# Kernel tuning notes

Hardware: AMD Instinct MI355X
Metric: run time of the kernel (lower is better)

The kernel has to match this reference:

```python
import jax, jax.numpy as jnp
import numpy as np

EPS = 1e-5
KS = 3
PAD = 1


def _bn(x, g, b, m, v):
    inv = g / jnp.sqrt(v + EPS)
    return x * inv[None, :, None, None] + (b - m * inv)[None, :, None, None]


def _deform_conv2d(x, off_w, off_b, w):
    # x: (B,C,H,W); off_w: (2*9,C,3,3); w: (Cout,C,3,3)
    B, C, H, W = x.shape
    N = KS * KS
    off = jax.lax.conv_general_dilated(x, off_w, (1, 1), ((PAD, PAD), (PAD, PAD)))
    off = off + off_b[None, :, None, None]                      # (B,2N,H,W)
    xp = jnp.pad(x, ((0, 0), (0, 0), (PAD, PAD), (PAD, PAD)))
    Hp, Wp = H + 2 * PAD, W + 2 * PAD
    r = jnp.arange(KS, dtype=x.dtype) - (KS - 1) // 2           # kernel offsets
    pny = jnp.repeat(r, KS)                                     # row-major (dy)
    pnx = jnp.tile(r, KS)                                       # row-major (dx)
    p0y = jnp.arange(1, H + 1, dtype=x.dtype)[None, None, :, None]
    p0x = jnp.arange(1, W + 1, dtype=x.dtype)[None, None, None, :]
    py = off[:, :N] + pny[None, :, None, None] + p0y            # (B,N,H,W)
    px = off[:, N:] + pnx[None, :, None, None] + p0x
    py = jnp.clip(py, 0.0, Hp - 1.0)
    px = jnp.clip(px, 0.0, Wp - 1.0)
    fy = jax.lax.stop_gradient(jnp.floor(py))                   # indices detached (as in torch impl)
    fx = jax.lax.stop_gradient(jnp.floor(px))
    qy0 = jnp.clip(fy, 0.0, Hp - 1.0)
    qx0 = jnp.clip(fx, 0.0, Wp - 1.0)
    qy1 = jnp.clip(fy + 1.0, 0.0, Hp - 1.0)
    qx1 = jnp.clip(fx + 1.0, 0.0, Wp - 1.0)
    xf = xp.reshape(B, C, Hp * Wp)

    def gather(qy, qx):
        idx = (qy * Wp + qx).astype(jnp.int32)                  # (B,N,H,W)
        return jax.vmap(lambda m_, i_: m_[:, i_])(xf, idx)       # (B,C,N,H,W)

    g_lt = (1.0 + (qy0 - py)) * (1.0 + (qx0 - px))
    g_rb = (1.0 - (qy1 - py)) * (1.0 - (qx1 - px))
    g_lb = (1.0 + (qy0 - py)) * (1.0 - (qx1 - px))
    g_rt = (1.0 - (qy1 - py)) * (1.0 + (qx0 - px))
    xo = (g_lt[:, None] * gather(qy0, qx0) + g_rb[:, None] * gather(qy1, qx1)
          + g_lb[:, None] * gather(qy0, qx1) + g_rt[:, None] * gather(qy1, qx0))
    # (B,C,N,H,W) -> (B,C,H*KS,W*KS): N = (row, col) row-major
    xo = xo.reshape(B, C, KS, KS, H, W).transpose(0, 1, 4, 2, 5, 3).reshape(B, C, H * KS, W * KS)
    return jax.lax.conv_general_dilated(xo, w, (KS, KS), 'VALID')


def _forward(x, dc1_offw, dc1_offb, dc1_w, bn1_g, bn1_b, bn1_m, bn1_v,
             dc2_offw, dc2_offb, dc2_w, bn2_g, bn2_b, bn2_m, bn2_v,
             id_w, id_b, bn3_g, bn3_b, bn3_m, bn3_v):
    h = jax.nn.relu(_bn(_deform_conv2d(x, dc1_offw, dc1_offb, dc1_w), bn1_g, bn1_b, bn1_m, bn1_v))
    h = _bn(_deform_conv2d(h, dc2_offw, dc2_offb, dc2_w), bn2_g, bn2_b, bn2_m, bn2_v)
    idt = jnp.einsum('bchw,oc->bohw', x, id_w[:, :, 0, 0]) + id_b[None, :, None, None]
    idt = _bn(idt, bn3_g, bn3_b, bn3_m, bn3_v)
    return jax.nn.relu(h + idt)


def setup_inputs() -> dict:
    key = jax.random.key(0)
    ks = jax.random.split(key, 16)
    B, Cin, Cout, H, W = 2, 64, 128, 128, 128
    N2 = 2 * KS * KS
    d = {}
    d['x'] = jax.random.normal(ks[0], (B, Cin, H, W), jnp.float32)
    d['dc1_offw'] = jax.random.normal(ks[1], (N2, Cin, KS, KS), jnp.float32) * 0.01
    d['dc1_offb'] = jnp.zeros((N2,), jnp.float32)
    d['dc1_w'] = jax.random.normal(ks[2], (Cout, Cin, KS, KS), jnp.float32) * 0.05
    d['bn1_g'] = 1.0 + 0.1 * jax.random.normal(ks[3], (Cout,), jnp.float32)
    d['bn1_b'] = 0.1 * jax.random.normal(ks[4], (Cout,), jnp.float32)
    d['bn1_m'] = 0.1 * jax.random.normal(ks[5], (Cout,), jnp.float32)
    d['bn1_v'] = jnp.ones((Cout,), jnp.float32)
    d['dc2_offw'] = jax.random.normal(ks[6], (N2, Cout, KS, KS), jnp.float32) * 0.01
    d['dc2_offb'] = jnp.zeros((N2,), jnp.float32)
    d['dc2_w'] = jax.random.normal(ks[7], (Cout, Cout, KS, KS), jnp.float32) * 0.03
    d['bn2_g'] = 1.0 + 0.1 * jax.random.normal(ks[8], (Cout,), jnp.float32)
    d['bn2_b'] = 0.1 * jax.random.normal(ks[9], (Cout,), jnp.float32)
    d['bn2_m'] = 0.1 * jax.random.normal(ks[10], (Cout,), jnp.float32)
    d['bn2_v'] = jnp.ones((Cout,), jnp.float32)
    d['id_w'] = jax.random.normal(ks[11], (Cout, Cin, 1, 1), jnp.float32) * 0.1
    d['id_b'] = jnp.zeros((Cout,), jnp.float32)
    d['bn3_g'] = 1.0 + 0.1 * jax.random.normal(ks[12], (Cout,), jnp.float32)
    d['bn3_b'] = 0.1 * jax.random.normal(ks[13], (Cout,), jnp.float32)
    d['bn3_m'] = 0.1 * jax.random.normal(ks[14], (Cout,), jnp.float32)
    d['bn3_v'] = jnp.ones((Cout,), jnp.float32)
    return d


def reference(x, dc1_offw, dc1_offb, dc1_w, bn1_g, bn1_b, bn1_m, bn1_v,
              dc2_offw, dc2_offb, dc2_w, bn2_g, bn2_b, bn2_m, bn2_v,
              id_w, id_b, bn3_g, bn3_b, bn3_m, bn3_v):
    return _forward(x, dc1_offw, dc1_offb, dc1_w, bn1_g, bn1_b, bn1_m, bn1_v,
                    dc2_offw, dc2_offb, dc2_w, bn2_g, bn2_b, bn2_m, bn2_v,
                    id_w, id_b, bn3_g, bn3_b, bn3_m, bn3_v)
```

## Files before the change

kernel.cpp:

```cpp
#include <hip/hip_runtime.h>
#include <math.h>

#define HH 128
#define WW 128
#define HWSZ (HH * WW)
#define BB 2
#define COUT 128

typedef __bf16 bf16x8 __attribute__((ext_vector_type(8)));
typedef float f32x4 __attribute__((ext_vector_type(4)));
typedef float f32x2 __attribute__((ext_vector_type(2)));
typedef short s16x8 __attribute__((ext_vector_type(8)));
typedef short s16x4 __attribute__((ext_vector_type(4)));
typedef unsigned short u16x4 __attribute__((ext_vector_type(4)));
typedef unsigned short u16x8 __attribute__((ext_vector_type(8)));

__device__ __forceinline__ short tobf(float f) {
  union { float f; unsigned u; } v; v.f = f;
  unsigned r = v.u + 0x7fffu + ((v.u >> 16) & 1u);
  return (short)(r >> 16);
}
__device__ __forceinline__ float asf(unsigned u) {
  union { unsigned u; float f; } v; v.u = u;
  return v.f;
}
__device__ __forceinline__ f32x2 up2(unsigned u) {
  f32x2 r; r[0] = asf(u << 16); r[1] = asf(u & 0xffff0000u); return r;
}
__device__ __forceinline__ unsigned pack2bf(float a, float b) {
  union { float f; unsigned u; } x, y; x.f = a; y.f = b;
  unsigned lo = (x.u + 0x7fffu + ((x.u >> 16) & 1u)) >> 16;
  unsigned hi = (y.u + 0x7fffu + ((y.u >> 16) & 1u)) & 0xffff0000u;
  return lo | hi;
}

#define PA0 73728
#define PA1 221184
#define PA2 229376
#define PA3 247808
#define PA4 284672
#define PA5 284928
__global__ __launch_bounds__(256) void prep_all_kernel(
    const float* __restrict__ dc1_w, const float* __restrict__ dc2_w,
    const float* __restrict__ id_w, const float* __restrict__ dc1_offw,
    const float* __restrict__ dc2_offw,
    const float* g1, const float* b1, const float* m1, const float* v1,
    const float* g2, const float* b2, const float* m2, const float* v2,
    const float* g3, const float* b3, const float* m3, const float* v3,
    const float* idb,
    short* __restrict__ wbf1, short* __restrict__ wbf2,
    short* __restrict__ woff1, short* __restrict__ woff2,
    float* __restrict__ cb1, float* __restrict__ cb2) {
  int idx = blockIdx.x * 256 + threadIdx.x;
  if (idx < PA0) {
    int o = idx / 576, k = idx - o * 576;
    float inv = g1[o] / sqrtf(v1[o] + 1e-5f);
    int col = (k % 9) * 64 + k / 9;
    wbf1[o * 576 + col] = tobf(dc1_w[(size_t)o * 576 + k] * inv);
  } else if (idx < PA1) {
    int j = idx - PA0;
    int o = j / 1152, k = j - o * 1152;
    float inv = g2[o] / sqrtf(v2[o] + 1e-5f);
    int col = (k % 9) * 128 + k / 9;
    wbf2[o * 1216 + col] = tobf(dc2_w[(size_t)o * 1152 + k] * inv);
  } else if (idx < PA2) {
    int j = idx - PA1;
    int o = j >> 6, k = j & 63;
    float inv = g3[o] / sqrtf(v3[o] + 1e-5f);
    wbf2[o * 1216 + 1152 + k] = tobf(id_w[(size_t)o * 64 + k] * inv);
  } else if (idx < PA3) {
    int j = idx - PA2;
    int o = j / 576, k = j - o * 576;
    int col = (k % 9) * 64 + k / 9;
    woff1[o * 576 + col] = (o < 18) ? tobf(dc1_offw[(size_t)o * 576 + k]) : (short)0;
  } else if (idx < PA4) {
    int j = idx - PA3;
    int o = j / 1152, k = j - o * 1152;
    int col = (k % 9) * 128 + k / 9;
    woff2[o * 1152 + col] = (o < 18) ? tobf(dc2_offw[(size_t)o * 1152 + k]) : (short)0;
  } else if (idx < PA5) {
    int j = idx - PA4;
    if (j < 128) {
      float inv = g1[j] / sqrtf(v1[j] + 1e-5f);
      cb1[j] = b1[j] - m1[j] * inv;
    } else {
      int o = j - 128;
      float inv2_ = g2[o] / sqrtf(v2[o] + 1e-5f);
      float inv3_ = g3[o] / sqrtf(v3[o] + 1e-5f);
      cb2[o] = (b2[o] - m2[o] * inv2_) + idb[o] * inv3_ + (b3[o] - m3[o] * inv3_);
    }
  }
}

__global__ __launch_bounds__(256) void xcast_kernel(const float* __restrict__ x,
                                                    unsigned short* __restrict__ xn) {
  __shared__ short lds[64 * 72];
  int tid = threadIdx.x;
  int gp0 = blockIdx.x * 64;
  int b = gp0 >> 14;
  int pl0 = gp0 & 16383;
  int p = tid & 63;
  int cb = (tid >> 6) * 16;
#pragma unroll
  for (int i = 0; i < 16; i++) {
    int c = cb + i;
    lds[p * 72 + c] = tobf(x[((size_t)(b * 64 + c)) * HWSZ + pl0 + p]);
  }
  __syncthreads();
  int pw = tid >> 2, cseg = (tid & 3) * 16;
  u16x8 a = *(const u16x8*)&lds[pw * 72 + cseg];
  u16x8 b8 = *(const u16x8*)&lds[pw * 72 + cseg + 8];
  *(u16x8*)&xn[(size_t)(gp0 + pw) * 64 + cseg] = a;
  *(u16x8*)&xn[(size_t)(gp0 + pw) * 64 + cseg + 8] = b8;
}

__global__ __launch_bounds__(256, 8) void offconv_mfma_kernel(
    const unsigned short* __restrict__ in, const short* __restrict__ woff,
    const float* __restrict__ offb, float* __restrict__ off, int cshift) {
  __shared__ short wlds[2][32 * 40];
  __shared__ short vlds[2][32 * 40];
  const int tid = threadIdx.x;
  const int lane = tid & 63, wv = tid >> 6;
  const int pb = ((blockIdx.x & 7) << 7) | (blockIdx.x >> 3);
  const int pix0 = pb << 5;
  const int x0 = pix0 & 127, y = (pix0 >> 7) & 127, b = pix0 >> 14;
  const int Cin = 1 << cshift;
  const int Kc = 9 << cshift;
  const unsigned short* inb = in + (size_t)b * HWSZ * Cin;
  const int ps = tid >> 3, cq = tid & 7;
  const int l15 = lane & 15, quad = lane >> 4;
  const int ptile = wv & 1, otile = wv >> 1;

  s16x8 wreg;
  u16x4 pk;
  auto issue = [&](int k0) {
    if (tid < 128) wreg = *(const s16x8*)&woff[(size_t)(tid >> 2) * Kc + k0 + (tid & 3) * 8];
    int n = k0 >> cshift;
    int dy = n / 3 - 1, dx = n % 3 - 1;
    int yy = y + dy;
    int xx = x0 + ps + dx;
    int c0 = (k0 & (Cin - 1)) + cq * 4;
    pk = (u16x4){0, 0, 0, 0};
    if (((unsigned)yy < (unsigned)HH) && ((unsigned)xx < (unsigned)WW))
      pk = *(const u16x4*)&inb[((size_t)yy * WW + xx) * Cin + c0];
  };
  auto commit = [&](int buf) {
    if (tid < 128) *(s16x8*)&wlds[buf][(tid >> 2) * 40 + (tid & 3) * 8] = wreg;
    *(u16x4*)&vlds[buf][ps * 40 + cq * 4] = pk;
  };

  f32x4 acc = {0.f, 0.f, 0.f, 0.f};
  issue(0);
  commit(0);
  __syncthreads();
  const int NC = Kc >> 5;
  for (int ch = 0; ch < NC; ch++) {
    int cur = ch & 1;
    bool has = (ch + 1) < NC;
    if (has) issue((ch + 1) << 5);
    bf16x8 bfr = *(const bf16x8*)&vlds[cur][(ptile * 16 + l15) * 40 + quad * 8];
    bf16x8 afr = *(const bf16x8*)&wlds[cur][(otile * 16 + l15) * 40 + quad * 8];
    acc = __builtin_amdgcn_mfma_f32_16x16x32_bf16(afr, bfr, acc, 0, 0, 0);
    if (has) commit(cur ^ 1);
    __syncthreads();
  }
#pragma unroll
  for (int r = 0; r < 4; r++) {
    int o = otile * 16 + quad * 4 + r;
    if (o < 18)
      off[(size_t)(b * 18 + o) * HWSZ + y * WW + x0 + ptile * 16 + l15] = acc[r] + offb[o];
  }
}

__global__ __launch_bounds__(512, 4) void deform_mfma_kernel(
    const unsigned short* __restrict__ in, const float* __restrict__ off,
    const short* __restrict__ wbf, const float* __restrict__ cbv,
    const unsigned short* __restrict__ xid, float* __restrict__ outf,
    unsigned short* __restrict__ outb, int cshift, int KCONV, int KTOT, int mode) {
  __shared__ __align__(16) char smem[49152];
  float4* dw = (float4*)smem;
  int4* da = (int4*)(smem + 9216);
  short* wlds = (short*)(smem + 18432);
  short* vlds = (short*)(smem + 38912);
  short* trans = (short*)smem;

  const int tid = threadIdx.x;
  const int lane = tid & 63, wv = tid >> 6;
  const int pb = ((blockIdx.x & 7) << 6) | (blockIdx.x >> 3);
  const int pix0 = pb << 6;
  const int x0 = pix0 & 127, y = (pix0 >> 7) & 127, b = pix0 >> 14;
  const int Cin = 1 << cshift;
  const unsigned short* inb = in + (size_t)b * HWSZ * Cin;
  const int ps = tid >> 3, cq = tid & 7;
  const int l15 = lane & 15, quad = lane >> 4;
  const int ptile = wv & 3, og = wv >> 2;

  for (int t = tid; t < 576; t += 512) {
    int n = t >> 6, pp = t & 63;
    float offy = off[(size_t)(b * 18 + n) * HWSZ + y * WW + x0 + pp];
    float offx = off[(size_t)(b * 18 + 9 + n) * HWSZ + y * WW + x0 + pp];
    float py = offy + (float)(n / 3 - 1) + (float)(y + 1);
    float px = offx + (float)(n % 3 - 1) + (float)(x0 + pp + 1);
    py = fminf(fmaxf(py, 0.f), 129.f);
    px = fminf(fmaxf(px, 0.f), 129.f);
    float fy = floorf(py), fx = floorf(px);
    float qy1 = fminf(fy + 1.f, 129.f), qx1 = fminf(fx + 1.f, 129.f);
    float ty0 = 1.f + fy - py, ty1 = 1.f - (qy1 - py);
    float tx0 = 1.f + fx - px, tx1 = 1.f - (qx1 - px);
    int iy0 = (int)fy - 1, ix0 = (int)fx - 1;
    int iy1 = (int)qy1 - 1, ix1 = (int)qx1 - 1;
    if ((unsigned)iy0 >= (unsigned)HH) ty0 = 0.f;
    if ((unsigned)iy1 >= (unsigned)HH) ty1 = 0.f;
    if ((unsigned)ix0 >= (unsigned)WW) tx0 = 0.f;
    if ((unsigned)ix1 >= (unsigned)WW) tx1 = 0.f;
    int by0 = min(max(iy0, 0), HH - 1), by1 = min(max(iy1, 0), HH - 1);
    int bx0 = min(max(ix0, 0), WW - 1), bx1 = min(max(ix1, 0), WW - 1);
    dw[t] = make_float4(ty0 * tx0, ty0 * tx1, ty1 * tx0, ty1 * tx1);
    da[t] = make_int4((by0 * WW + bx0) * Cin, (bx1 - bx0) * Cin,
                      (by1 - by0) * WW * Cin, 0);
  }

  f32x4 acc[4];
#pragma unroll
  for (int i = 0; i < 4; i++) acc[i] = (f32x4){0.f, 0.f, 0.f, 0.f};

  s16x8 wreg;
  uint2 t00, t01, t10, t11, pkr;
  float4 wgt;
  int isres = 0;

  auto issue = [&](int k0) {
    wreg = *(const s16x8*)&wbf[(size_t)(tid >> 2) * KTOT + k0 + (tid & 3) * 8];
    if (k0 < KCONV) {
      isres = 0;
      int n = k0 >> cshift;
      int c0 = (k0 & (Cin - 1)) + cq * 4;
      int d = (n << 6) + ps;
      wgt = dw[d];
      int4 a = da[d];
      const unsigned short* ptr = inb + a.x + c0;
      t00 = *(const uint2*)(ptr);
      t01 = *(const uint2*)(ptr + a.y);
      t10 = *(const uint2*)(ptr + a.z);
      t11 = *(const uint2*)(ptr + a.y + a.z);
    } else {
      isres = 1;
      int c = k0 - KCONV + cq * 4;
      pkr = *(const uint2*)&xid[((size_t)(b * HWSZ) + y * WW + x0 + ps) * 64 + c];
    }
  };
  auto commit = [&](int buf) {
    uint2 pk;
    if (!isres) {
      f32x2 v0 = up2(t00.x) * wgt.x + up2(t01.x) * wgt.y
               + up2(t10.x) * wgt.z + up2(t11.x) * wgt.w;
      f32x2 v1 = up2(t00.y) * wgt.x + up2(t01.y) * wgt.y
               + up2(t10.y) * wgt.z + up2(t11.y) * wgt.w;
      pk.x = pack2bf(v0[0], v0[1]);
      pk.y = pack2bf(v1[0], v1[1]);
    } else {
      pk = pkr;
    }
    *(s16x8*)&wlds[buf * 5120 + (tid >> 2) * 40 + (tid & 3) * 8] = wreg;
    *(uint2*)&vlds[buf * 2560 + ps * 40 + cq * 4] = pk;
  };

  __syncthreads();
  issue(0);
  commit(0);
  __syncthreads();
  const int NC = KTOT >> 5;
  for (int ch = 0; ch < NC; ch++) {
    int cur = ch & 1;
    bool has = (ch + 1) < NC;
    if (has) issue((ch + 1) << 5);
    bf16x8 bfr = *(const bf16x8*)&vlds[cur * 2560 + (ptile * 16 + l15) * 40 + quad * 8];
#pragma unroll
    for (int ot = 0; ot < 4; ot++) {
      bf16x8 afr = *(const bf16x8*)&wlds[cur * 5120 + (og * 64 + ot * 16 + l15) * 40 + quad * 8];
      acc[ot] = __builtin_amdgcn_mfma_f32_16x16x32_bf16(afr, bfr, acc[ot], 0, 0, 0);
    }
    if (has) commit(cur ^ 1);
    __syncthreads();
  }

  if (mode == 1) {
    int px_ = x0 + ptile * 16 + l15;
#pragma unroll
    for (int ot = 0; ot < 4; ot++) {
#pragma unroll
      for (int r = 0; r < 4; r++) {
        int o = og * 64 + ot * 16 + quad * 4 + r;
        outf[(size_t)(b * COUT + o) * HWSZ + y * WW + px_] =
            fmaxf(acc[ot][r] + cbv[o], 0.f);
      }
    }
  } else {
    int pl = ptile * 16 + l15;
#pragma unroll
    for (int ot = 0; ot < 4; ot++) {
      s16x4 t4;
#pragma unroll
      for (int r = 0; r < 4; r++) {
        int o = og * 64 + ot * 16 + quad * 4 + r;
        t4[r] = tobf(fmaxf(acc[ot][r] + cbv[o], 0.f));
      }
      *(s16x4*)&trans[pl * 136 + og * 64 + ot * 16 + quad * 4] = t4;
    }
    __syncthreads();
    int pw = tid >> 3, cseg = (tid & 7) * 16;
    u16x8 a = *(const u16x8*)&trans[pw * 136 + cseg];
    u16x8 b8 = *(const u16x8*)&trans[pw * 136 + cseg + 8];
    size_t gb = ((size_t)(b * HWSZ) + y * WW + x0 + pw) * 128 + cseg;
    *(u16x8*)&outb[gb] = a;
    *(u16x8*)&outb[gb + 8] = b8;
  }
}

extern "C" void kernel_launch(void* const* d_in, const int* in_sizes, int n_in,
                              void* d_out, int out_size, void* d_ws, size_t ws_size,
                              hipStream_t stream) {
  const float* x        = (const float*)d_in[0];
  const float* dc1_offw = (const float*)d_in[1];
  const float* dc1_offb = (const float*)d_in[2];
  const float* dc1_w    = (const float*)d_in[3];
  const float* bn1_g    = (const float*)d_in[4];
  const float* bn1_b    = (const float*)d_in[5];
  const float* bn1_m    = (const float*)d_in[6];
  const float* bn1_v    = (const float*)d_in[7];
  const float* dc2_offw = (const float*)d_in[8];
  const float* dc2_offb = (const float*)d_in[9];
  const float* dc2_w    = (const float*)d_in[10];
  const float* bn2_g    = (const float*)d_in[11];
  const float* bn2_b    = (const float*)d_in[12];
  const float* bn2_m    = (const float*)d_in[13];
  const float* bn2_v    = (const float*)d_in[14];
  const float* id_w     = (const float*)d_in[15];
  const float* id_b     = (const float*)d_in[16];
  const float* bn3_g    = (const float*)d_in[17];
  const float* bn3_b    = (const float*)d_in[18];
  const float* bn3_m    = (const float*)d_in[19];
  const float* bn3_v    = (const float*)d_in[20];

  float* wsf = (float*)d_ws;
  float* off1 = wsf;
  float* off2 = off1 + (size_t)BB * 18 * HWSZ;
  float* cb1  = off2 + (size_t)BB * 18 * HWSZ;
  float* cb2  = cb1 + 128;
  unsigned short* xbf = (unsigned short*)(cb2 + 128);
  unsigned short* h1  = xbf + (size_t)BB * HWSZ * 64;
  short* wbf1  = (short*)(h1 + (size_t)BB * HWSZ * COUT);
  short* wbf2  = wbf1 + (size_t)128 * 576;
  short* woff1 = wbf2 + (size_t)128 * 1216;
  short* woff2 = woff1 + (size_t)32 * 576;

  const int K1 = 576, K2 = 1152, KT2 = 1216;

  hipLaunchKernelGGL(prep_all_kernel, dim3((PA5 + 255) / 256), dim3(256), 0, stream,
                     dc1_w, dc2_w, id_w, dc1_offw, dc2_offw,
                     bn1_g, bn1_b, bn1_m, bn1_v, bn2_g, bn2_b, bn2_m, bn2_v,
                     bn3_g, bn3_b, bn3_m, bn3_v, id_b,
                     wbf1, wbf2, woff1, woff2, cb1, cb2);
  hipLaunchKernelGGL(xcast_kernel, dim3(BB * HWSZ / 64), dim3(256), 0, stream, x, xbf);

  hipLaunchKernelGGL(offconv_mfma_kernel, dim3(1024), dim3(256), 0, stream,
                     xbf, woff1, dc1_offb, off1, 6);
  hipLaunchKernelGGL(deform_mfma_kernel, dim3(512), dim3(512), 0, stream,
                     xbf, off1, wbf1, cb1, (const unsigned short*)nullptr,
                     (float*)nullptr, h1, 6, K1, K1, 0);
  hipLaunchKernelGGL(offconv_mfma_kernel, dim3(1024), dim3(256), 0, stream,
                     h1, woff2, dc2_offb, off2, 7);
  hipLaunchKernelGGL(deform_mfma_kernel, dim3(512), dim3(512), 0, stream,
                     h1, off2, wbf2, cb2, xbf, (float*)d_out,
                     (unsigned short*)nullptr, 7, K2, KT2, 1);
}
```

Measured before the change: 195.7 us.

## Restructure offset conv with split-K and deform conv with full-row tiles

The offset conv kernel now reads weights directly from global memory in a pre-swizzled MFMA fragment layout and reads activations straight into registers, with no LDS staging. It splits K across two wave groups that are combined through a single LDS reduction. The deform conv kernel now processes a full 128-pixel row per block with 8-channel vector gathers, stores the bilinear weights as bf16 and the deltas as packed int2 to save LDS, and prefetches two stages ahead. This roughly doubles data reuse per block and cuts per-chunk synchronisation, but raises register use (launch bounds drop to 2 blocks per CU), halves the grid, and rounds the bilinear weights to bf16.

```diff
diff --git a/kernel.cpp b/kernel.cpp
--- a/kernel.cpp
+++ b/kernel.cpp
@@ -27,8 +27,8 @@
 __device__ __forceinline__ f32x2 up2(unsigned u) {
   f32x2 r; r[0] = asf(u << 16); r[1] = asf(u & 0xffff0000u); return r;
 }
-__device__ __forceinline__ unsigned pack2bf(float a, float b) {
-  union { float f; unsigned u; } x, y; x.f = a; y.f = b;
+__device__ __forceinline__ unsigned pack2bf(f32x2 v) {
+  union { float f; unsigned u; } x, y; x.f = v[0]; y.f = v[1];
   unsigned lo = (x.u + 0x7fffu + ((x.u >> 16) & 1u)) >> 16;
   unsigned hi = (y.u + 0x7fffu + ((y.u >> 16) & 1u)) & 0xffff0000u;
   return lo | hi;
@@ -72,12 +72,16 @@
     int j = idx - PA2;
     int o = j / 576, k = j - o * 576;
     int col = (k % 9) * 64 + k / 9;
-    woff1[o * 576 + col] = (o < 18) ? tobf(dc1_offw[(size_t)o * 576 + k]) : (short)0;
+    int di = ((col >> 5) * 2 + (o >> 4)) * 512 + ((col >> 3) & 3) * 128
+           + (o & 15) * 8 + (col & 7);
+    woff1[di] = (o < 18) ? tobf(dc1_offw[(size_t)o * 576 + k]) : (short)0;
   } else if (idx < PA4) {
     int j = idx - PA3;
     int o = j / 1152, k = j - o * 1152;
     int col = (k % 9) * 128 + k / 9;
-    woff2[o * 1152 + col] = (o < 18) ? tobf(dc2_offw[(size_t)o * 1152 + k]) : (short)0;
+    int di = ((col >> 5) * 2 + (o >> 4)) * 512 + ((col >> 3) & 3) * 128
+           + (o & 15) * 8 + (col & 7);
+    woff2[di] = (o < 18) ? tobf(dc2_offw[(size_t)o * 1152 + k]) : (short)0;
   } else if (idx < PA5) {
     int j = idx - PA4;
     if (j < 128) {
@@ -114,93 +118,90 @@
   *(u16x8*)&xn[(size_t)(gp0 + pw) * 64 + cseg + 8] = b8;
 }
 
-__global__ __launch_bounds__(256, 8) void offconv_mfma_kernel(
+__global__ __launch_bounds__(512, 4) void offconv_mfma_kernel(
     const unsigned short* __restrict__ in, const short* __restrict__ woff,
     const float* __restrict__ offb, float* __restrict__ off, int cshift) {
-  __shared__ short wlds[2][32 * 40];
-  __shared__ short vlds[2][32 * 40];
+  __shared__ float redf[4 * 64 * 8];
   const int tid = threadIdx.x;
   const int lane = tid & 63, wv = tid >> 6;
-  const int pb = ((blockIdx.x & 7) << 7) | (blockIdx.x >> 3);
-  const int pix0 = pb << 5;
+  const int pxg = wv & 3, kh = wv >> 2;
+  const int pb = ((blockIdx.x & 7) << 6) | (blockIdx.x >> 3);
+  const int pix0 = pb << 6;
   const int x0 = pix0 & 127, y = (pix0 >> 7) & 127, b = pix0 >> 14;
   const int Cin = 1 << cshift;
-  const int Kc = 9 << cshift;
+  const int HK = (9 << cshift) >> 1;
+  const int NCh = HK >> 5;
   const unsigned short* inb = in + (size_t)b * HWSZ * Cin;
-  const int ps = tid >> 3, cq = tid & 7;
   const int l15 = lane & 15, quad = lane >> 4;
-  const int ptile = wv & 1, otile = wv >> 1;
-
-  s16x8 wreg;
-  u16x4 pk;
-  auto issue = [&](int k0) {
-    if (tid < 128) wreg = *(const s16x8*)&woff[(size_t)(tid >> 2) * Kc + k0 + (tid & 3) * 8];
+  const int px = x0 + pxg * 16 + l15;
+
+  f32x4 acc[2];
+  acc[0] = (f32x4){0.f, 0.f, 0.f, 0.f};
+  acc[1] = (f32x4){0.f, 0.f, 0.f, 0.f};
+
+  for (int i = 0; i < NCh; i++) {
+    int k0 = kh * HK + i * 32;
     int n = k0 >> cshift;
-    int dy = n / 3 - 1, dx = n % 3 - 1;
-    int yy = y + dy;
-    int xx = x0 + ps + dx;
-    int c0 = (k0 & (Cin - 1)) + cq * 4;
-    pk = (u16x4){0, 0, 0, 0};
+    int c0 = (k0 & (Cin - 1)) + quad * 8;
+    int yy = y + n / 3 - 1;
+    int xx = px + n % 3 - 1;
+    bf16x8 bv = {};
     if (((unsigned)yy < (unsigned)HH) && ((unsigned)xx < (unsigned)WW))
-      pk = *(const u16x4*)&inb[((size_t)yy * WW + xx) * Cin + c0];
-  };
-  auto commit = [&](int buf) {
-    if (tid < 128) *(s16x8*)&wlds[buf][(tid >> 2) * 40 + (tid & 3) * 8] = wreg;
-    *(u16x4*)&vlds[buf][ps * 40 + cq * 4] = pk;
-  };
-
-  f32x4 acc = {0.f, 0.f, 0.f, 0.f};
-  issue(0);
-  commit(0);
+      bv = *(const bf16x8*)&inb[((size_t)yy * WW + xx) * Cin + c0];
+    int fbase = (k0 >> 5) * 1024 + lane * 8;
+    bf16x8 a0 = *(const bf16x8*)&woff[fbase];
+    bf16x8 a1 = *(const bf16x8*)&woff[fbase + 512];
+    acc[0] = __builtin_amdgcn_mfma_f32_16x16x32_bf16(a0, bv, acc[0], 0, 0, 0);
+    acc[1] = __builtin_amdgcn_mfma_f32_16x16x32_bf16(a1, bv, acc[1], 0, 0, 0);
+  }
+  if (kh == 1) {
+    *(f32x4*)&redf[(pxg * 64 + lane) * 8] = acc[0];
+    *(f32x4*)&redf[(pxg * 64 + lane) * 8 + 4] = acc[1];
+  }
   __syncthreads();
-  const int NC = Kc >> 5;
-  for (int ch = 0; ch < NC; ch++) {
-    int cur = ch & 1;
-    bool has = (ch + 1) < NC;
-    if (has) issue((ch + 1) << 5);
-    bf16x8 bfr = *(const bf16x8*)&vlds[cur][(ptile * 16 + l15) * 40 + quad * 8];
-    bf16x8 afr = *(const bf16x8*)&wlds[cur][(otile * 16 + l15) * 40 + quad * 8];
-    acc = __builtin_amdgcn_mfma_f32_16x16x32_bf16(afr, bfr, acc, 0, 0, 0);
-    if (has) commit(cur ^ 1);
-    __syncthreads();
-  }
-#pragma unroll
-  for (int r = 0; r < 4; r++) {
-    int o = otile * 16 + quad * 4 + r;
-    if (o < 18)
-      off[(size_t)(b * 18 + o) * HWSZ + y * WW + x0 + ptile * 16 + l15] = acc[r] + offb[o];
-  }
-}
-
-__global__ __launch_bounds__(512, 4) void deform_mfma_kernel(
+  if (kh == 0) {
+    acc[0] += *(const f32x4*)&redf[(pxg * 64 + lane) * 8];
+    acc[1] += *(const f32x4*)&redf[(pxg * 64 + lane) * 8 + 4];
+#pragma unroll
+    for (int ot = 0; ot < 2; ot++) {
+#pragma unroll
+      for (int r = 0; r < 4; r++) {
+        int o = ot * 16 + quad * 4 + r;
+        if (o < 18)
+          off[(size_t)(b * 18 + o) * HWSZ + y * WW + px] = acc[ot][r] + offb[o];
+      }
+    }
+  }
+}
+
+__global__ __launch_bounds__(512, 2) void deform_mfma_kernel(
     const unsigned short* __restrict__ in, const float* __restrict__ off,
     const short* __restrict__ wbf, const float* __restrict__ cbv,
     const unsigned short* __restrict__ xid, float* __restrict__ outf,
     unsigned short* __restrict__ outb, int cshift, int KCONV, int KTOT, int mode) {
-  __shared__ __align__(16) char smem[49152];
-  float4* dw = (float4*)smem;
-  int4* da = (int4*)(smem + 9216);
+  __shared__ __align__(16) char smem[59392];
+  u16x4* dsw = (u16x4*)smem;
+  int2* dsa = (int2*)(smem + 9216);
   short* wlds = (short*)(smem + 18432);
   short* vlds = (short*)(smem + 38912);
   short* trans = (short*)smem;
 
   const int tid = threadIdx.x;
   const int lane = tid & 63, wv = tid >> 6;
-  const int pb = ((blockIdx.x & 7) << 6) | (blockIdx.x >> 3);
-  const int pix0 = pb << 6;
-  const int x0 = pix0 & 127, y = (pix0 >> 7) & 127, b = pix0 >> 14;
+  const int pb = ((blockIdx.x & 7) << 5) | (blockIdx.x >> 3);
+  const int y = pb & 127, b = pb >> 7;
   const int Cin = 1 << cshift;
   const unsigned short* inb = in + (size_t)b * HWSZ * Cin;
-  const int ps = tid >> 3, cq = tid & 7;
+  const int ps = tid >> 2, cq = tid & 3;
   const int l15 = lane & 15, quad = lane >> 4;
-  const int ptile = wv & 3, og = wv >> 2;
-
-  for (int t = tid; t < 576; t += 512) {
-    int n = t >> 6, pp = t & 63;
-    float offy = off[(size_t)(b * 18 + n) * HWSZ + y * WW + x0 + pp];
-    float offx = off[(size_t)(b * 18 + 9 + n) * HWSZ + y * WW + x0 + pp];
+  const int pxq = wv & 3, oh = wv >> 2;
+
+  for (int t = tid; t < 9 * 128; t += 512) {
+    int n = t >> 7, pp = t & 127;
+    float offy = off[(size_t)(b * 18 + n) * HWSZ + y * WW + pp];
+    float offx = off[(size_t)(b * 18 + 9 + n) * HWSZ + y * WW + pp];
     float py = offy + (float)(n / 3 - 1) + (float)(y + 1);
-    float px = offx + (float)(n % 3 - 1) + (float)(x0 + pp + 1);
+    float px = offx + (float)(n % 3 - 1) + (float)(pp + 1);
     py = fminf(fmaxf(py, 0.f), 129.f);
     px = fminf(fmaxf(px, 0.f), 129.f);
     float fy = floorf(py), fx = floorf(px);
@@ -215,105 +216,128 @@
     if ((unsigned)ix1 >= (unsigned)WW) tx1 = 0.f;
     int by0 = min(max(iy0, 0), HH - 1), by1 = min(max(iy1, 0), HH - 1);
     int bx0 = min(max(ix0, 0), WW - 1), bx1 = min(max(ix1, 0), WW - 1);
-    dw[t] = make_float4(ty0 * tx0, ty0 * tx1, ty1 * tx0, ty1 * tx1);
-    da[t] = make_int4((by0 * WW + bx0) * Cin, (bx1 - bx0) * Cin,
-                      (by1 - by0) * WW * Cin, 0);
-  }
-
-  f32x4 acc[4];
-#pragma unroll
-  for (int i = 0; i < 4; i++) acc[i] = (f32x4){0.f, 0.f, 0.f, 0.f};
-
-  s16x8 wreg;
-  uint2 t00, t01, t10, t11, pkr;
-  float4 wgt;
-  int isres = 0;
-
-  auto issue = [&](int k0) {
-    wreg = *(const s16x8*)&wbf[(size_t)(tid >> 2) * KTOT + k0 + (tid & 3) * 8];
+    u16x4 w4;
+    w4[0] = (unsigned short)tobf(ty0 * tx0);
+    w4[1] = (unsigned short)tobf(ty0 * tx1);
+    w4[2] = (unsigned short)tobf(ty1 * tx0);
+    w4[3] = (unsigned short)tobf(ty1 * tx1);
+    dsw[t] = w4;
+    dsa[t] = make_int2((by0 * WW + bx0) * Cin,
+                       (((by1 - by0) * WW * Cin) << 16) | ((bx1 - bx0) * Cin));
+  }
+
+  f32x4 acc[2][4];
+#pragma unroll
+  for (int i = 0; i < 2; i++)
+#pragma unroll
+    for (int j = 0; j < 4; j++) acc[i][j] = (f32x4){0.f, 0.f, 0.f, 0.f};
+
+  s16x8 wr[2];
+  uint4 t00[2], t01[2], t10[2], t11[2];
+  u16x4 wq[2];
+  int isres[2];
+
+  auto issue = [&](int k0, int s) {
+    wr[s] = *(const s16x8*)&wbf[(size_t)ps * KTOT + k0 + cq * 8];
     if (k0 < KCONV) {
-      isres = 0;
+      isres[s] = 0;
       int n = k0 >> cshift;
-      int c0 = (k0 & (Cin - 1)) + cq * 4;
-      int d = (n << 6) + ps;
-      wgt = dw[d];
-      int4 a = da[d];
-      const unsigned short* ptr = inb + a.x + c0;
-      t00 = *(const uint2*)(ptr);
-      t01 = *(const uint2*)(ptr + a.y);
-      t10 = *(const uint2*)(ptr + a.z);
-      t11 = *(const uint2*)(ptr + a.y + a.z);
+      int c0 = (k0 & (Cin - 1)) + cq * 8;
+      int d = (n << 7) + ps;
+      wq[s] = dsw[d];
+      int2 ai = dsa[d];
+      int dx = ai.y & 0xffff, dy = ai.y >> 16;
+      const unsigned short* ptr = inb + ai.x + c0;
+      t00[s] = *(const uint4*)(ptr);
+      t01[s] = *(const uint4*)(ptr + dx);
+      t10[s] = *(const uint4*)(ptr + dy);
+      t11[s] = *(const uint4*)(ptr + dx + dy);
     } else {
-      isres = 1;
-      int c = k0 - KCONV + cq * 4;
-      pkr = *(const uint2*)&xid[((size_t)(b * HWSZ) + y * WW + x0 + ps) * 64 + c];
+      isres[s] = 1;
+      int c = k0 - KCONV + cq * 8;
+      t00[s] = *(const uint4*)&xid[((size_t)(b * HWSZ) + y * WW + ps) * 64 + c];
     }
   };
-  auto commit = [&](int buf) {
-    uint2 pk;
-    if (!isres) {
-      f32x2 v0 = up2(t00.x) * wgt.x + up2(t01.x) * wgt.y
-               + up2(t10.x) * wgt.z + up2(t11.x) * wgt.w;
-      f32x2 v1 = up2(t00.y) * wgt.x + up2(t01.y) * wgt.y
-               + up2(t10.y) * wgt.z + up2(t11.y) * wgt.w;
-      pk.x = pack2bf(v0[0], v0[1]);
-      pk.y = pack2bf(v1[0], v1[1]);
+  auto commit = [&](int buf, int s) {
+    uint4 pk;
+    if (!isres[s]) {
+      float w0 = asf((unsigned)wq[s][0] << 16), w1 = asf((unsigned)wq[s][1] << 16);
+      float w2 = asf((unsigned)wq[s][2] << 16), w3 = asf((unsigned)wq[s][3] << 16);
+      f32x2 v0 = up2(t00[s].x) * w0 + up2(t01[s].x) * w1
+               + up2(t10[s].x) * w2 + up2(t11[s].x) * w3;
+      f32x2 v1 = up2(t00[s].y) * w0 + up2(t01[s].y) * w1
+               + up2(t10[s].y) * w2 + up2(t11[s].y) * w3;
+      f32x2 v2 = up2(t00[s].z) * w0 + up2(t01[s].z) * w1
+               + up2(t10[s].z) * w2 + up2(t11[s].z) * w3;
+      f32x2 v3 = up2(t00[s].w) * w0 + up2(t01[s].w) * w1
+               + up2(t10[s].w) * w2 + up2(t11[s].w) * w3;
+      pk.x = pack2bf(v0); pk.y = pack2bf(v1); pk.z = pack2bf(v2); pk.w = pack2bf(v3);
     } else {
-      pk = pkr;
-    }
-    *(s16x8*)&wlds[buf * 5120 + (tid >> 2) * 40 + (tid & 3) * 8] = wreg;
-    *(uint2*)&vlds[buf * 2560 + ps * 40 + cq * 4] = pk;
+      pk = t00[s];
+    }
+    *(s16x8*)&wlds[buf * 5120 + ps * 40 + cq * 8] = wr[s];
+    *(uint4*)&vlds[buf * 5120 + ps * 40 + cq * 8] = pk;
   };
 
-  __syncthreads();
-  issue(0);
-  commit(0);
   __syncthreads();
   const int NC = KTOT >> 5;
+  issue(0, 0);
+  commit(0, 0);
+  if (NC > 1) issue(32, 1);
+  __syncthreads();
+
   for (int ch = 0; ch < NC; ch++) {
     int cur = ch & 1;
-    bool has = (ch + 1) < NC;
-    if (has) issue((ch + 1) << 5);
-    bf16x8 bfr = *(const bf16x8*)&vlds[cur * 2560 + (ptile * 16 + l15) * 40 + quad * 8];
+    if (ch + 2 < NC) issue((ch + 2) << 5, ch & 1);
+    bf16x8 bf0 = *(const bf16x8*)&vlds[cur * 5120 + (pxq * 32 + l15) * 40 + quad * 8];
+    bf16x8 bf1 = *(const bf16x8*)&vlds[cur * 5120 + (pxq * 32 + 16 + l15) * 40 + quad * 8];
 #pragma unroll
     for (int ot = 0; ot < 4; ot++) {
-      bf16x8 afr = *(const bf16x8*)&wlds[cur * 5120 + (og * 64 + ot * 16 + l15) * 40 + quad * 8];
-      acc[ot] = __builtin_amdgcn_mfma_f32_16x16x32_bf16(afr, bfr, acc[ot], 0, 0, 0);
-    }
-    if (has) commit(cur ^ 1);
+      bf16x8 afr = *(const bf16x8*)&wlds[cur * 5120 + (oh * 64 + ot * 16 + l15) * 40 + quad * 8];
+      acc[0][ot] = __builtin_amdgcn_mfma_f32_16x16x32_bf16(afr, bf0, acc[0][ot], 0, 0, 0);
+      acc[1][ot] = __builtin_amdgcn_mfma_f32_16x16x32_bf16(afr, bf1, acc[1][ot], 0, 0, 0);
+    }
+    if (ch + 1 < NC) commit(cur ^ 1, (ch + 1) & 1);
     __syncthreads();
   }
 
   if (mode == 1) {
-    int px_ = x0 + ptile * 16 + l15;
-#pragma unroll
-    for (int ot = 0; ot < 4; ot++) {
-#pragma unroll
-      for (int r = 0; r < 4; r++) {
-        int o = og * 64 + ot * 16 + quad * 4 + r;
-        outf[(size_t)(b * COUT + o) * HWSZ + y * WW + px_] =
-            fmaxf(acc[ot][r] + cbv[o], 0.f);
+#pragma unroll
+    for (int pxi = 0; pxi < 2; pxi++) {
+      int px_ = pxq * 32 + pxi * 16 + l15;
+#pragma unroll
+      for (int ot = 0; ot < 4; ot++) {
+#pragma unroll
+        for (int r = 0; r < 4; r++) {
+          int o = oh * 64 + ot * 16 + quad * 4 + r;
+          outf[(size_t)(b * COUT + o) * HWSZ + y * WW + px_] =
+              fmaxf(acc[pxi][ot][r] + cbv[o], 0.f);
+        }
       }
     }
   } else {
-    int pl = ptile * 16 + l15;
-#pragma unroll
-    for (int ot = 0; ot < 4; ot++) {
-      s16x4 t4;
-#pragma unroll
-      for (int r = 0; r < 4; r++) {
-        int o = og * 64 + ot * 16 + quad * 4 + r;
-        t4[r] = tobf(fmaxf(acc[ot][r] + cbv[o], 0.f));
+#pragma unroll
+    for (int pxi = 0; pxi < 2; pxi++) {
+      int px_ = pxq * 32 + pxi * 16 + l15;
+#pragma unroll
+      for (int ot = 0; ot < 4; ot++) {
+        s16x4 t4;
+#pragma unroll
+        for (int r = 0; r < 4; r++) {
+          int o = oh * 64 + ot * 16 + quad * 4 + r;
+          t4[r] = tobf(fmaxf(acc[pxi][ot][r] + cbv[o], 0.f));
+        }
+        *(s16x4*)&trans[px_ * 136 + oh * 64 + ot * 16 + quad * 4] = t4;
       }
-      *(s16x4*)&trans[pl * 136 + og * 64 + ot * 16 + quad * 4] = t4;
     }
     __syncthreads();
-    int pw = tid >> 3, cseg = (tid & 7) * 16;
-    u16x8 a = *(const u16x8*)&trans[pw * 136 + cseg];
-    u16x8 b8 = *(const u16x8*)&trans[pw * 136 + cseg + 8];
-    size_t gb = ((size_t)(b * HWSZ) + y * WW + x0 + pw) * 128 + cseg;
-    *(u16x8*)&outb[gb] = a;
-    *(u16x8*)&outb[gb + 8] = b8;
+    int pw = tid >> 2, cs = (tid & 3) * 32;
+    size_t gb = ((size_t)(b * HWSZ) + y * WW + pw) * 128 + cs;
+#pragma unroll
+    for (int i = 0; i < 4; i++) {
+      u16x8 v8 = *(const u16x8*)&trans[pw * 136 + cs + i * 8];
+      *(u16x8*)&outb[gb + i * 8] = v8;
+    }
   }
 }
 
@@ -352,7 +376,7 @@
   short* wbf1  = (short*)(h1 + (size_t)BB * HWSZ * COUT);
   short* wbf2  = wbf1 + (size_t)128 * 576;
   short* woff1 = wbf2 + (size_t)128 * 1216;
-  short* woff2 = woff1 + (size_t)32 * 576;
+  short* woff2 = woff1 + (size_t)18 * 1024;
 
   const int K1 = 576, K2 = 1152, KT2 = 1216;
 
@@ -363,14 +387,14 @@
                      wbf1, wbf2, woff1, woff2, cb1, cb2);
   hipLaunchKernelGGL(xcast_kernel, dim3(BB * HWSZ / 64), dim3(256), 0, stream, x, xbf);
 
-  hipLaunchKernelGGL(offconv_mfma_kernel, dim3(1024), dim3(256), 0, stream,
+  hipLaunchKernelGGL(offconv_mfma_kernel, dim3(512), dim3(512), 0, stream,
                      xbf, woff1, dc1_offb, off1, 6);
-  hipLaunchKernelGGL(deform_mfma_kernel, dim3(512), dim3(512), 0, stream,
+  hipLaunchKernelGGL(deform_mfma_kernel, dim3(256), dim3(512), 0, stream,
                      xbf, off1, wbf1, cb1, (const unsigned short*)nullptr,
                      (float*)nullptr, h1, 6, K1, K1, 0);
-  hipLaunchKernelGGL(offconv_mfma_kernel, dim3(1024), dim3(256), 0, stream,
+  hipLaunchKernelGGL(offconv_mfma_kernel, dim3(512), dim3(512), 0, stream,
                      h1, woff2, dc2_offb, off2, 7);
-  hipLaunchKernelGGL(deform_mfma_kernel, dim3(512), dim3(512), 0, stream,
+  hipLaunchKernelGGL(deform_mfma_kernel, dim3(256), dim3(512), 0, stream,
                      h1, off2, wbf2, cb2, xbf, (float*)d_out,
                      (unsigned short*)nullptr, 7, K2, KT2, 1);
 }
```

After: 415.4 us. 2.12x slower.
